# Optimization experiments

Measured on AMD Instinct MI355X. Metric: run time of the kernel, lower is better.

## Reference

```python
import jax, jax.numpy as jnp
import numpy as np

F_DIM = 128
H_DIM = 128
T_DIM = H_DIM // 4          # 32
D = H_DIM + T_DIM           # 160, block hidden dim
N_NODES = 100000
N_EDGES = 800000
N_LAYERS = 2
LN_EPS = 1e-5


def _layernorm(x, g, b):
    m = jnp.mean(x, axis=-1, keepdims=True)
    v = jnp.mean(jnp.square(x - m), axis=-1, keepdims=True)
    return (x - m) * jax.lax.rsqrt(v + LN_EPS) * g + b


def setup_inputs() -> dict:
    key = jax.random.key(0)
    ks = jax.random.split(key, 24)
    p = lambda k, shape: jax.random.normal(k, shape, dtype=jnp.float32) * 0.05
    inp = {
        "node_features": jax.random.normal(ks[0], (N_NODES, F_DIM), dtype=jnp.float32),
        "edge_index": jax.random.randint(ks[1], (2, N_EDGES), 0, N_NODES, dtype=jnp.int32),
        "edge_weights": jax.random.uniform(ks[2], (N_EDGES,), dtype=jnp.float32),
        "time_steps": jax.random.uniform(ks[3], (N_NODES, 1), dtype=jnp.float32),
        # node encoder: Linear(F,H) + LN(H)
        "w_enc": p(ks[4], (H_DIM, F_DIM)), "b_enc": jnp.zeros((H_DIM,)),
        "g_enc": jnp.ones((H_DIM,)), "be_enc": jnp.zeros((H_DIM,)),
        # time encoder: Linear(1,T) + LN(T)
        "w_time": p(ks[5], (T_DIM, 1)), "b_time": jnp.zeros((T_DIM,)),
        "g_time": jnp.ones((T_DIM,)), "be_time": jnp.zeros((T_DIM,)),
        # per-layer block params (stacked over layers)
        "wm": p(ks[6], (N_LAYERS, D, 2 * D)), "bm": jnp.zeros((N_LAYERS, D)),
        "gm": jnp.ones((N_LAYERS, D)), "bem": jnp.zeros((N_LAYERS, D)),
        "wu": p(ks[7], (N_LAYERS, D, 2 * D)), "bu": jnp.zeros((N_LAYERS, D)),
        "gu": jnp.ones((N_LAYERS, D)), "beu": jnp.zeros((N_LAYERS, D)),
        "wg": p(ks[8], (N_LAYERS, 1, D)), "bg": jnp.zeros((N_LAYERS, 1)),
        # output projection Linear(D, F)
        "w_out": p(ks[9], (F_DIM, D)), "b_out": jnp.zeros((F_DIM,)),
    }
    return inp


def _block(h, src, dst, w, wm, bm, gm, bem, wu, bu, gu, beu, wg, bg):
    n = h.shape[0]
    # gather endpoints -> per-edge message MLP -> weight -> scatter-add mean
    ecat = jnp.concatenate([h[src], h[dst]], axis=-1)              # [E, 2D]
    em = jax.nn.relu(_layernorm(ecat @ wm.T + bm, gm, bem)) * w[:, None]
    msum = jax.ops.segment_sum(em, dst, num_segments=n)            # [N, D]
    cnt = jax.ops.segment_sum(jnp.ones_like(w), dst, num_segments=n)[:, None]
    valid = (cnt > 0).astype(h.dtype)
    messages = msum / (cnt + 1e-8) * valid
    tw = jax.nn.sigmoid(h @ wg.T + bg)                             # [N, 1]
    h_new = jax.nn.relu(_layernorm(jnp.concatenate([h, messages], axis=-1) @ wu.T + bu, gu, beu))
    return tw * h_new + (1 - tw) * h


def reference(node_features, edge_index, edge_weights, time_steps,
              w_enc, b_enc, g_enc, be_enc, w_time, b_time, g_time, be_time,
              wm, bm, gm, bem, wu, bu, gu, beu, wg, bg, w_out, b_out):
    src, dst = edge_index[0], edge_index[1]
    h = jax.nn.relu(_layernorm(node_features @ w_enc.T + b_enc, g_enc, be_enc))
    t = jax.nn.relu(_layernorm(time_steps @ w_time.T + b_time, g_time, be_time))
    h_t = jnp.concatenate([h, t], axis=-1)                          # [N, D]
    for l in range(N_LAYERS):
        h_t = _block(h_t, src, dst, edge_weights,
                     wm[l], bm[l], gm[l], bem[l],
                     wu[l], bu[l], gu[l], beu[l], wg[l], bg[l])
    out = h_t @ w_out.T + b_out
    # F.normalize(dim=-1), eps=1e-12
    norm = jnp.linalg.norm(out, axis=-1, keepdims=True)
    return out / jnp.maximum(norm, 1e-12)
```

## Files before the change

kernel.cpp:

```cpp
#include <hip/hip_runtime.h>

#define NN 100000
#define NE 800000

typedef _Float16 half8 __attribute__((ext_vector_type(8)));
typedef _Float16 half4 __attribute__((ext_vector_type(4)));
typedef float floatx4 __attribute__((ext_vector_type(4)));

#define LDB(Wf, f) (*(const half8*)&(Wf)[(f) * 512])

__global__ __launch_bounds__(256) void k_zero(float4* __restrict__ p, int n4) {
  int i = blockIdx.x * 256 + threadIdx.x;
  if (i < n4) p[i] = make_float4(0.f, 0.f, 0.f, 0.f);
}

__global__ __launch_bounds__(256) void k_pack(
    const float* __restrict__ w_enc, const float* __restrict__ w_out,
    const float* __restrict__ wu, const float* __restrict__ wm,
    _Float16* __restrict__ WeP, _Float16* __restrict__ WoP,
    _Float16* __restrict__ WuP, _Float16* __restrict__ WpP) {
  int gid = blockIdx.x * 256 + threadIdx.x;
  int fid = gid >> 6, lane = gid & 63;
  int mrow = lane & 15, quad = lane >> 4;
  const float* src; _Float16* dst; int stride, NI, f, g;
  if (fid < 32) {
    f = fid; g = f; src = w_enc; dst = WeP; stride = 128; NI = 8;
  } else if (fid < 72) {
    f = fid - 32; g = f; src = w_out; dst = WoP; stride = 160; NI = 8;
  } else if (fid < 272) {
    f = fid - 72; g = f % 100; src = wu + (f / 100) * 51200; dst = WuP; stride = 320; NI = 10;
  } else {
    f = fid - 272; g = f % 50;
    int l = f / 100, h = (f % 100) / 50;
    src = wm + l * 51200 + h * 160; dst = WpP; stride = 320; NI = 10;
  }
  int kk = g / NI, i = g - kk * NI;
  const float* sp = src + (size_t)(i * 16 + mrow) * stride + kk * 32 + quad * 8;
  float4 f0 = *(const float4*)sp;
  float4 f1 = *(const float4*)(sp + 4);
  half8 v = {(_Float16)f0.x, (_Float16)f0.y, (_Float16)f0.z, (_Float16)f0.w,
             (_Float16)f1.x, (_Float16)f1.y, (_Float16)f1.z, (_Float16)f1.w};
  *(half8*)&dst[(size_t)(f * 64 + lane) * 8] = v;
}

__global__ __launch_bounds__(256) void k_count_i(const int* __restrict__ ei,
                                                 int* __restrict__ cnti) {
  int e = blockIdx.x * 256 + threadIdx.x;
  atomicAdd(&cnti[ei[NE + e]], 1);
}

__global__ __launch_bounds__(256) void k_scan1(const int* __restrict__ cnti,
                                               int* __restrict__ off,
                                               int* __restrict__ bsum) {
  __shared__ int sh[256];
  const int t = threadIdx.x;
  const int i = blockIdx.x * 256 + t;
  int v = (i < NN) ? cnti[i] : 0;
  sh[t] = v;
  __syncthreads();
  for (int d = 1; d < 256; d <<= 1) {
    int add = (t >= d) ? sh[t - d] : 0;
    __syncthreads();
    sh[t] += add;
    __syncthreads();
  }
  if (i < NN) off[i] = sh[t] - v;
  if (t == 255) bsum[blockIdx.x] = sh[255];
}

__global__ __launch_bounds__(512) void k_scan2(const int* __restrict__ bsum,
                                               int* __restrict__ bsum2) {
  __shared__ int sh[512];
  const int t = threadIdx.x;
  int v = (t < 391) ? bsum[t] : 0;
  sh[t] = v;
  __syncthreads();
  for (int d = 1; d < 512; d <<= 1) {
    int add = (t >= d) ? sh[t - d] : 0;
    __syncthreads();
    sh[t] += add;
    __syncthreads();
  }
  if (t < 391) bsum2[t] = sh[t] - v;
}

__global__ __launch_bounds__(256) void k_scan3(int* __restrict__ off,
                                               const int* __restrict__ bsum2,
                                               int* __restrict__ cursor) {
  const int i = blockIdx.x * 256 + threadIdx.x;
  if (i < NN) {
    int o = off[i] + bsum2[blockIdx.x];
    off[i] = o;
    cursor[i] = o;
  }
  if (i == 0) off[NN] = NE;
}

__global__ __launch_bounds__(256) void k_scatter(const int* __restrict__ ei,
                                                 const float* __restrict__ ew,
                                                 int* __restrict__ cursor,
                                                 int2* __restrict__ selist) {
  int e = blockIdx.x * 256 + threadIdx.x;
  int dst = ei[NE + e];
  int pos = atomicAdd(&cursor[dst], 1);
  selist[pos] = make_int2(ei[e], __float_as_int(ew[e]));
}

__device__ __forceinline__ half8 cvt8(const float* p) {
  float4 f0 = *(const float4*)p;
  float4 f1 = *(const float4*)(p + 4);
  half8 a = {(_Float16)f0.x, (_Float16)f0.y, (_Float16)f0.z, (_Float16)f0.w,
             (_Float16)f1.x, (_Float16)f1.y, (_Float16)f1.z, (_Float16)f1.w};
  return a;
}

__device__ __forceinline__ void write_h16_wave(_Float16* __restrict__ h16,
                                               const _Float16* tile, int n0,
                                               int w, int lane) {
#pragma unroll
  for (int u = 0; u < 5; ++u) {
    int c = lane + u * 64;
    int row = c / 20, col = (c - row * 20) * 8;
    int node = n0 + w * 16 + row;
    if (node < NN)
      *(half8*)&h16[(size_t)node * 160 + col] = *(const half8*)&tile[(w * 16 + row) * 168 + col];
  }
}

__device__ __forceinline__ void phase2_proj(
    const _Float16* __restrict__ WpP, const float* __restrict__ bm,
    _Float16* __restrict__ P, const _Float16* tile,
    int lane, int w, int mrow, int quad, int n0) {
#pragma unroll 1
  for (int half_ = 0; half_ < 2; ++half_) {
    const _Float16* Wf = WpP + half_ * 25600 + lane * 8;
    floatx4 acc2[10];
#pragma unroll
    for (int i = 0; i < 10; ++i) acc2[i] = (floatx4)0.f;
#pragma unroll
    for (int kk = 0; kk < 5; ++kk) {
      half8 a = *(const half8*)&tile[(w * 16 + mrow) * 168 + kk * 32 + quad * 8];
#pragma unroll
      for (int i = 0; i < 10; ++i) {
        half8 b = LDB(Wf, kk * 10 + i);
        acc2[i] = __builtin_amdgcn_mfma_f32_16x16x32_f16(a, b, acc2[i], 0, 0, 0);
      }
    }
#pragma unroll
    for (int r = 0; r < 4; ++r) {
      const int row = quad * 4 + r;
      const int node = n0 + w * 16 + row;
      if (node < NN) {
        _Float16* prow = &P[(size_t)node * 320 + half_ * 160];
#pragma unroll
        for (int i = 0; i < 10; ++i) {
          int jj = i * 16 + mrow;
          prow[jj] = (_Float16)(acc2[i][r] + (half_ ? bm[jj] : 0.f));
        }
      }
    }
  }
}

__global__ __launch_bounds__(128, 4) void k_encode_proj(
    const float* __restrict__ x, const float* __restrict__ tsp,
    const _Float16* __restrict__ WeP,
    const float* __restrict__ b_enc, const float* __restrict__ g_enc,
    const float* __restrict__ be_enc,
    const float* __restrict__ w_time, const float* __restrict__ b_time,
    const float* __restrict__ g_time, const float* __restrict__ be_time,
    const _Float16* __restrict__ WpP, const float* __restrict__ bm,
    _Float16* __restrict__ h16, _Float16* __restrict__ P) {
  __shared__ _Float16 tile[32 * 168];
  const int t = threadIdx.x;
  const int lane = t & 63, w = t >> 6;
  const int mrow = lane & 15, quad = lane >> 4;
  const int n0 = blockIdx.x * 32;
  int arow = n0 + w * 16 + mrow; if (arow > NN - 1) arow = NN - 1;
  const float* xrow = x + (size_t)arow * 128;
  half8 areg[4];
#pragma unroll
  for (int kt = 0; kt < 4; ++kt) areg[kt] = cvt8(&xrow[kt * 32 + quad * 8]);
  float mw = 0.f, mb = 0.f;
  for (int d = 0; d < 32; ++d) { mw += w_time[d]; mb += b_time[d]; }
  mw *= (1.f / 32.f); mb *= (1.f / 32.f);
  float A = 0.f, B = 0.f, C = 0.f;
  for (int d = 0; d < 32; ++d) {
    float a = w_time[d] - mw, c = b_time[d] - mb;
    A = fmaf(a, a, A); B = fmaf(a, c, B); C = fmaf(c, c, C);
  }
  A *= (1.f / 32.f); B *= (1.f / 32.f); C *= (1.f / 32.f);
  floatx4 acc[8];
#pragma unroll
  for (int i = 0; i < 8; ++i) acc[i] = (floatx4)0.f;
  const _Float16* Wf = WeP + lane * 8;
#pragma unroll
  for (int kk = 0; kk < 4; ++kk) {
    half8 a = areg[kk];
#pragma unroll
    for (int i = 0; i < 8; ++i) {
      half8 b = LDB(Wf, kk * 8 + i);
      acc[i] = __builtin_amdgcn_mfma_f32_16x16x32_f16(a, b, acc[i], 0, 0, 0);
    }
  }
#pragma unroll
  for (int r = 0; r < 4; ++r) {
    const int row = quad * 4 + r;
    float v[8], s = 0.f, ss = 0.f;
#pragma unroll
    for (int i = 0; i < 8; ++i) {
      v[i] = acc[i][r] + b_enc[i * 16 + mrow];
      s += v[i]; ss = fmaf(v[i], v[i], ss);
    }
#pragma unroll
    for (int off = 1; off < 16; off <<= 1) { s += __shfl_xor(s, off); ss += __shfl_xor(ss, off); }
    const float m = s * (1.f / 128.f);
    const float rs = rsqrtf(ss * (1.f / 128.f) - m * m + 1e-5f);
#pragma unroll
    for (int i = 0; i < 8; ++i) {
      int j = i * 16 + mrow;
      tile[(w * 16 + row) * 168 + j] =
          (_Float16)fmaxf(fmaf((v[i] - m) * rs, g_enc[j], be_enc[j]), 0.f);
    }
  }
#pragma unroll
  for (int rr = 0; rr < 8; ++rr) {
    int q = lane + rr * 64;
    int nn = q >> 5, d = q & 31;
    int node = n0 + w * 16 + nn;
    int nodec = (node > NN - 1) ? NN - 1 : node;
    float tsv = tsp[nodec];
    float mt = fmaf(mw, tsv, mb);
    float rst = rsqrtf(fmaf(fmaf(A, tsv, 2.f * B), tsv, C) + 1e-5f);
    float vv = fmaf(w_time[d], tsv, b_time[d]);
    float y = fmaxf(fmaf((vv - mt) * rst, g_time[d], be_time[d]), 0.f);
    tile[(w * 16 + nn) * 168 + 128 + d] = (_Float16)y;
  }
  write_h16_wave(h16, tile, n0, w, lane);
  phase2_proj(WpP, bm, P, tile, lane, w, mrow, quad, n0);
}

__global__ __launch_bounds__(256) void k_edge3(
    const _Float16* __restrict__ P, const int* __restrict__ off,
    const int2* __restrict__ selist,
    const float* __restrict__ gm, const float* __restrict__ bem,
    _Float16* __restrict__ msum16) {
  const int t = threadIdx.x;
  const int jg = t & 31, g = t >> 5;
  const int n = blockIdx.x * 8 + g;
  float gmv[5], bev[5], pdv[5];
#pragma unroll
  for (int i = 0; i < 4; ++i) { gmv[i] = gm[4 * jg + i]; bev[i] = bem[4 * jg + i]; }
  gmv[4] = gm[128 + jg]; bev[4] = bem[128 + jg];
  const _Float16* pd = P + (size_t)n * 320 + 160;
  half4 pdh = *(const half4*)&pd[4 * jg];
  pdv[0] = (float)pdh.x; pdv[1] = (float)pdh.y; pdv[2] = (float)pdh.z; pdv[3] = (float)pdh.w;
  pdv[4] = (float)pd[128 + jg];
  float acc[5] = {0.f, 0.f, 0.f, 0.f, 0.f};
  const int e0 = off[n], e1 = off[n + 1];
  int k = e0;
  for (; k + 1 < e1; k += 2) {
    int2 seA = selist[k], seB = selist[k + 1];
    const _Float16* psA = P + (size_t)seA.x * 320;
    const _Float16* psB = P + (size_t)seB.x * 320;
    const float weA = __int_as_float(seA.y), weB = __int_as_float(seB.y);
    half4 a4 = *(const half4*)&psA[4 * jg];
    half4 b4 = *(const half4*)&psB[4 * jg];
    float a5 = (float)psA[128 + jg], b5 = (float)psB[128 + jg];
    float vA[5], vB[5];
    vA[0] = (float)a4.x + pdv[0]; vA[1] = (float)a4.y + pdv[1];
    vA[2] = (float)a4.z + pdv[2]; vA[3] = (float)a4.w + pdv[3]; vA[4] = a5 + pdv[4];
    vB[0] = (float)b4.x + pdv[0]; vB[1] = (float)b4.y + pdv[1];
    vB[2] = (float)b4.z + pdv[2]; vB[3] = (float)b4.w + pdv[3]; vB[4] = b5 + pdv[4];
    float sA = 0.f, ssA = 0.f, sB = 0.f, ssB = 0.f;
#pragma unroll
    for (int i = 0; i < 5; ++i) {
      sA += vA[i]; ssA = fmaf(vA[i], vA[i], ssA);
      sB += vB[i]; ssB = fmaf(vB[i], vB[i], ssB);
    }
#pragma unroll
    for (int o = 1; o < 32; o <<= 1) {
      sA += __shfl_xor(sA, o); ssA += __shfl_xor(ssA, o);
      sB += __shfl_xor(sB, o); ssB += __shfl_xor(ssB, o);
    }
    const float mA = sA * (1.f / 160.f), mB = sB * (1.f / 160.f);
    const float rsA = rsqrtf(ssA * (1.f / 160.f) - mA * mA + 1e-5f);
    const float rsB = rsqrtf(ssB * (1.f / 160.f) - mB * mB + 1e-5f);
#pragma unroll
    for (int i = 0; i < 5; ++i) {
      acc[i] = fmaf(fmaxf(fmaf((vA[i] - mA) * rsA, gmv[i], bev[i]), 0.f), weA, acc[i]);
      acc[i] = fmaf(fmaxf(fmaf((vB[i] - mB) * rsB, gmv[i], bev[i]), 0.f), weB, acc[i]);
    }
  }
  if (k < e1) {
    int2 se = selist[k];
    const _Float16* ps = P + (size_t)se.x * 320;
    const float we = __int_as_float(se.y);
    half4 s4 = *(const half4*)&ps[4 * jg];
    float v[5], s = 0.f, ss = 0.f;
    v[0] = (float)s4.x + pdv[0]; v[1] = (float)s4.y + pdv[1];
    v[2] = (float)s4.z + pdv[2]; v[3] = (float)s4.w + pdv[3];
    v[4] = (float)ps[128 + jg] + pdv[4];
#pragma unroll
    for (int i = 0; i < 5; ++i) { s += v[i]; ss = fmaf(v[i], v[i], ss); }
#pragma unroll
    for (int o = 1; o < 32; o <<= 1) { s += __shfl_xor(s, o); ss += __shfl_xor(ss, o); }
    const float m = s * (1.f / 160.f);
    const float rs = rsqrtf(ss * (1.f / 160.f) - m * m + 1e-5f);
#pragma unroll
    for (int i = 0; i < 5; ++i)
      acc[i] = fmaf(fmaxf(fmaf((v[i] - m) * rs, gmv[i], bev[i]), 0.f), we, acc[i]);
  }
  const float c = (float)(e1 - e0);
  const float ic = (c > 0.f) ? 1.f / (c + 1e-8f) : 0.f;
  _Float16* orow = msum16 + (size_t)n * 160;
  half4 o4 = {(_Float16)(acc[0] * ic), (_Float16)(acc[1] * ic),
              (_Float16)(acc[2] * ic), (_Float16)(acc[3] * ic)};
  *(half4*)&orow[4 * jg] = o4;
  orow[128 + jg] = (_Float16)(acc[4] * ic);
}

__device__ __forceinline__ void update_phase1(
    const _Float16* __restrict__ h16, const _Float16* __restrict__ msum16,
    const _Float16* __restrict__ WuP, const float* __restrict__ bu,
    const float* __restrict__ gu, const float* __restrict__ beu,
    const float* __restrict__ wg, const float* __restrict__ bg,
    _Float16* tile, int lane, int w, int mrow, int quad, int n0) {
  int arow = n0 + w * 16 + mrow; if (arow > NN - 1) arow = NN - 1;
  const _Float16* hrowp = h16 + (size_t)arow * 160;
  const _Float16* mrowp = msum16 + (size_t)arow * 160;
  half8 areg[10];
#pragma unroll
  for (int kt = 0; kt < 5; ++kt) areg[kt] = *(const half8*)&hrowp[kt * 32 + quad * 8];
#pragma unroll
  for (int kt = 5; kt < 10; ++kt) areg[kt] = *(const half8*)&mrowp[kt * 32 + quad * 8 - 160];
  float gp = 0.f;
#pragma unroll
  for (int kt = 0; kt < 5; ++kt) {
    const int k0 = kt * 32 + quad * 8;
    float4 g0 = *(const float4*)&wg[k0];
    float4 g1 = *(const float4*)&wg[k0 + 4];
    gp = fmaf((float)areg[kt][0], g0.x, gp); gp = fmaf((float)areg[kt][1], g0.y, gp);
    gp = fmaf((float)areg[kt][2], g0.z, gp); gp = fmaf((float)areg[kt][3], g0.w, gp);
    gp = fmaf((float)areg[kt][4], g1.x, gp); gp = fmaf((float)areg[kt][5], g1.y, gp);
    gp = fmaf((float)areg[kt][6], g1.z, gp); gp = fmaf((float)areg[kt][7], g1.w, gp);
  }
  gp += __shfl_xor(gp, 16); gp += __shfl_xor(gp, 32);
  const float twv = 1.f / (1.f + expf(-(gp + bg[0])));
  floatx4 acc[10];
#pragma unroll
  for (int i = 0; i < 10; ++i) acc[i] = (floatx4)0.f;
  const _Float16* Wf = WuP + lane * 8;
#pragma unroll
  for (int kk = 0; kk < 10; ++kk) {
    half8 a = areg[kk];
#pragma unroll
    for (int i = 0; i < 10; ++i) {
      half8 b = LDB(Wf, kk * 10 + i);
      acc[i] = __builtin_amdgcn_mfma_f32_16x16x32_f16(a, b, acc[i], 0, 0, 0);
    }
  }
#pragma unroll
  for (int r = 0; r < 4; ++r) {
    const int row = quad * 4 + r;
    const int node = n0 + w * 16 + row;
    const int nodec = (node > NN - 1) ? NN - 1 : node;
    float v[10], s = 0.f, ss = 0.f;
#pragma unroll
    for (int i = 0; i < 10; ++i) {
      v[i] = acc[i][r] + bu[i * 16 + mrow];
      s += v[i]; ss = fmaf(v[i], v[i], ss);
    }
#pragma unroll
    for (int off = 1; off < 16; off <<= 1) { s += __shfl_xor(s, off); ss += __shfl_xor(ss, off); }
    const float m = s * (1.f / 160.f);
    const float rs = rsqrtf(ss * (1.f / 160.f) - m * m + 1e-5f);
    const float g = __shfl(twv, row);
    const _Float16* hr = h16 + (size_t)nodec * 160;
#pragma unroll
    for (int i = 0; i < 10; ++i) {
      int j = i * 16 + mrow;
      float hnew = fmaxf(fmaf((v[i] - m) * rs, gu[j], beu[j]), 0.f);
      float hold = (float)hr[j];
      tile[(w * 16 + row) * 168 + j] = (_Float16)fmaf(g, hnew - hold, hold);
    }
  }
}

__global__ __launch_bounds__(128, 4) void k_update_proj(
    _Float16* __restrict__ h16, const _Float16* __restrict__ msum16,
    const _Float16* __restrict__ WuP, const float* __restrict__ bu,
    const float* __restrict__ gu, const float* __restrict__ beu,
    const float* __restrict__ wg, const float* __restrict__ bg,
    const _Float16* __restrict__ WpP, const float* __restrict__ bm,
    _Float16* __restrict__ P) {
  __shared__ _Float16 tile[32 * 168];
  const int t = threadIdx.x;
  const int lane = t & 63, w = t >> 6;
  const int mrow = lane & 15, quad = lane >> 4;
  const int n0 = blockIdx.x * 32;
  update_phase1(h16, msum16, WuP, bu, gu, beu, wg, bg, tile, lane, w, mrow, quad, n0);
  write_h16_wave(h16, tile, n0, w, lane);
  phase2_proj(WpP, bm, P, tile, lane, w, mrow, quad, n0);
}

__global__ __launch_bounds__(128, 4) void k_update_out(
    const _Float16* __restrict__ h16, const _Float16* __restrict__ msum16,
    const _Float16* __restrict__ WuP, const float* __restrict__ bu,
    const float* __restrict__ gu, const float* __restrict__ beu,
    const float* __restrict__ wg, const float* __restrict__ bg,
    const _Float16* __restrict__ WoP, const float* __restrict__ b_out,
    float* __restrict__ out) {
  __shared__ _Float16 tile[32 * 168];
  const int t = threadIdx.x;
  const int lane = t & 63, w = t >> 6;
  const int mrow = lane & 15, quad = lane >> 4;
  const int n0 = blockIdx.x * 32;
  update_phase1(h16, msum16, WuP, bu, gu, beu, wg, bg, tile, lane, w, mrow, quad, n0);
  floatx4 acc2[8];
#pragma unroll
  for (int i = 0; i < 8; ++i) acc2[i] = (floatx4)0.f;
  const _Float16* Wf2 = WoP + lane * 8;
#pragma unroll
  for (int kk = 0; kk < 5; ++kk) {
    half8 a = *(const half8*)&tile[(w * 16 + mrow) * 168 + kk * 32 + quad * 8];
#pragma unroll
    for (int i = 0; i < 8; ++i) {
      half8 b = LDB(Wf2, kk * 8 + i);
      acc2[i] = __builtin_amdgcn_mfma_f32_16x16x32_f16(a, b, acc2[i], 0, 0, 0);
    }
  }
#pragma unroll
  for (int r = 0; r < 4; ++r) {
    const int row = quad * 4 + r;
    const int node = n0 + w * 16 + row;
    float v[8], ss = 0.f;
#pragma unroll
    for (int i = 0; i < 8; ++i) {
      v[i] = acc2[i][r] + b_out[i * 16 + mrow];
      ss = fmaf(v[i], v[i], ss);
    }
#pragma unroll
    for (int off = 1; off < 16; off <<= 1) ss += __shfl_xor(ss, off);
    const float inv = 1.f / fmaxf(sqrtf(ss), 1e-12f);
    if (node < NN) {
#pragma unroll
      for (int i = 0; i < 8; ++i)
        out[(size_t)node * 128 + i * 16 + mrow] = v[i] * inv;
    }
  }
}

extern "C" void kernel_launch(void* const* d_in, const int* in_sizes, int n_in,
                              void* d_out, int out_size, void* d_ws, size_t ws_size,
                              hipStream_t stream) {
  (void)in_sizes; (void)n_in; (void)out_size; (void)ws_size;
  const float* x       = (const float*)d_in[0];
  const int*   ei      = (const int*)  d_in[1];
  const float* ew      = (const float*)d_in[2];
  const float* tsp     = (const float*)d_in[3];
  const float* w_enc   = (const float*)d_in[4];
  const float* b_enc   = (const float*)d_in[5];
  const float* g_enc   = (const float*)d_in[6];
  const float* be_enc  = (const float*)d_in[7];
  const float* w_time  = (const float*)d_in[8];
  const float* b_time  = (const float*)d_in[9];
  const float* g_time  = (const float*)d_in[10];
  const float* be_time = (const float*)d_in[11];
  const float* wm      = (const float*)d_in[12];
  const float* bm      = (const float*)d_in[13];
  const float* gm      = (const float*)d_in[14];
  const float* bem     = (const float*)d_in[15];
  const float* wu      = (const float*)d_in[16];
  const float* bu      = (const float*)d_in[17];
  const float* gu      = (const float*)d_in[18];
  const float* beu     = (const float*)d_in[19];
  const float* wg      = (const float*)d_in[20];
  const float* bg      = (const float*)d_in[21];
  const float* w_out   = (const float*)d_in[22];
  const float* b_out   = (const float*)d_in[23];
  float* out = (float*)d_out;

  char* ws = (char*)d_ws;
  _Float16* h16    = (_Float16*)ws;
  _Float16* msum16 = (_Float16*)(ws + 32000000);
  _Float16* P      = (_Float16*)(ws + 64000000);
  _Float16* WuP16  = (_Float16*)(ws + 128000000);
  _Float16* WoP16  = (_Float16*)(ws + 128204800);
  char* ob = (char*)d_out;
  _Float16* WpP16 = (_Float16*)ob;
  _Float16* WeP16 = (_Float16*)(ob + 204800);
  int* off    = (int*)(ob + 237568);
  int* cnti   = (int*)(ob + 637584);
  int* cursor = (int*)(ob + 1037584);
  int* bsum   = (int*)(ob + 1437584);
  int* bsum2  = (int*)(ob + 1439152);
  int2* selist = (int2*)(ob + 1440720);

  k_zero<<<dim3(98), dim3(256), 0, stream>>>((float4*)cnti, 25000);
  k_pack<<<dim3(118), dim3(256), 0, stream>>>(w_enc, w_out, wu, wm,
                                              WeP16, WoP16, WuP16, WpP16);
  k_count_i<<<dim3(3125), dim3(256), 0, stream>>>(ei, cnti);
  k_scan1<<<dim3(391), dim3(256), 0, stream>>>(cnti, off, bsum);
  k_scan2<<<dim3(1), dim3(512), 0, stream>>>(bsum, bsum2);
  k_scan3<<<dim3(391), dim3(256), 0, stream>>>(off, bsum2, cursor);
  k_scatter<<<dim3(3125), dim3(256), 0, stream>>>(ei, ew, cursor, selist);

  k_encode_proj<<<dim3(3125), dim3(128), 0, stream>>>(
      x, tsp, WeP16, b_enc, g_enc, be_enc, w_time, b_time, g_time, be_time,
      WpP16, bm, h16, P);
  k_edge3<<<dim3(12500), dim3(256), 0, stream>>>(P, off, selist, gm, bem, msum16);
  k_update_proj<<<dim3(3125), dim3(128), 0, stream>>>(
      h16, msum16, WuP16, bu, gu, beu, wg, bg,
      WpP16 + 51200, bm + 160, P);
  k_edge3<<<dim3(12500), dim3(256), 0, stream>>>(P, off, selist, gm + 160, bem + 160, msum16);
  k_update_out<<<dim3(3125), dim3(128), 0, stream>>>(
      h16, msum16, WuP16 + 51200, bu + 160, gu + 160, beu + 160, wg + 160, bg + 1,
      WoP16, b_out, out);
}
```

Measured before the change: 555.0 us.

## Double-buffer weight fragments and shrink node kernels to one wave per block

The three node-level MFMA kernels now run 16 nodes per 64-thread block instead of 32 nodes per 128 threads, so each block is a single wave and uses half the shared tile. Their GEMM loops are rewritten to software-pipeline the B-fragment loads in groups of 4 or 5 with ping-pong register buffers, also prefetching the next GEMM's first weight group across phases. A-operand loads are streamed per k-step instead of being held all at once. This targets global-load latency stalls on the weights, at the cost of more live registers and dropped bounds checks, which are safe only because NN divides evenly by 16.

```diff
diff --git a/kernel.cpp b/kernel.cpp
--- a/kernel.cpp
+++ b/kernel.cpp
@@ -114,55 +114,68 @@
   return a;
 }
 
+__device__ __forceinline__ void ldg5(half8 d[5], const _Float16* Wf, int g) {
+#pragma unroll
+  for (int ii = 0; ii < 5; ++ii) d[ii] = LDB(Wf, g * 5 + ii);
+}
+__device__ __forceinline__ void ldg4(half8 d[4], const _Float16* Wf, int g) {
+#pragma unroll
+  for (int ii = 0; ii < 4; ++ii) d[ii] = LDB(Wf, g * 4 + ii);
+}
+
 __device__ __forceinline__ void write_h16_wave(_Float16* __restrict__ h16,
                                                const _Float16* tile, int n0,
-                                               int w, int lane) {
+                                               int lane) {
 #pragma unroll
   for (int u = 0; u < 5; ++u) {
     int c = lane + u * 64;
     int row = c / 20, col = (c - row * 20) * 8;
-    int node = n0 + w * 16 + row;
-    if (node < NN)
-      *(half8*)&h16[(size_t)node * 160 + col] = *(const half8*)&tile[(w * 16 + row) * 168 + col];
+    *(half8*)&h16[(size_t)(n0 + row) * 160 + col] = *(const half8*)&tile[row * 168 + col];
   }
 }
 
 __device__ __forceinline__ void phase2_proj(
     const _Float16* __restrict__ WpP, const float* __restrict__ bm,
-    _Float16* __restrict__ P, const _Float16* tile,
-    int lane, int w, int mrow, int quad, int n0) {
-#pragma unroll 1
+    _Float16* __restrict__ P, const _Float16* tile, half8 bA[5], half8 bB[5],
+    int lane, int mrow, int quad, int n0) {
+#pragma unroll
   for (int half_ = 0; half_ < 2; ++half_) {
     const _Float16* Wf = WpP + half_ * 25600 + lane * 8;
+    const _Float16* Wfn = WpP + 25600 + lane * 8;
     floatx4 acc2[10];
 #pragma unroll
     for (int i = 0; i < 10; ++i) acc2[i] = (floatx4)0.f;
-#pragma unroll
-    for (int kk = 0; kk < 5; ++kk) {
-      half8 a = *(const half8*)&tile[(w * 16 + mrow) * 168 + kk * 32 + quad * 8];
-#pragma unroll
-      for (int i = 0; i < 10; ++i) {
-        half8 b = LDB(Wf, kk * 10 + i);
-        acc2[i] = __builtin_amdgcn_mfma_f32_16x16x32_f16(a, b, acc2[i], 0, 0, 0);
+    half8 a_cur = *(const half8*)&tile[mrow * 168 + quad * 8];
+#pragma unroll
+    for (int g = 0; g < 10; ++g) {
+      half8* bc = (g & 1) ? bB : bA;
+      half8* bn = (g & 1) ? bA : bB;
+      if (g + 1 < 10) ldg5(bn, Wf, g + 1);
+      else if (half_ == 0) ldg5(bn, Wfn, 0);
+      half8 a_use = a_cur;
+      if ((g & 1) && g < 9) {
+        int kk1 = (g + 1) >> 1;
+        a_cur = *(const half8*)&tile[mrow * 168 + kk1 * 32 + quad * 8];
       }
+      const int ib = (g & 1) * 5;
+#pragma unroll
+      for (int ii = 0; ii < 5; ++ii)
+        acc2[ib + ii] = __builtin_amdgcn_mfma_f32_16x16x32_f16(a_use, bc[ii], acc2[ib + ii], 0, 0, 0);
     }
 #pragma unroll
     for (int r = 0; r < 4; ++r) {
       const int row = quad * 4 + r;
-      const int node = n0 + w * 16 + row;
-      if (node < NN) {
-        _Float16* prow = &P[(size_t)node * 320 + half_ * 160];
-#pragma unroll
-        for (int i = 0; i < 10; ++i) {
-          int jj = i * 16 + mrow;
-          prow[jj] = (_Float16)(acc2[i][r] + (half_ ? bm[jj] : 0.f));
-        }
+      _Float16* prow = &P[(size_t)(n0 + row) * 320 + half_ * 160];
+#pragma unroll
+      for (int i = 0; i < 10; ++i) {
+        int jj = i * 16 + mrow;
+        prow[jj] = (_Float16)(acc2[i][r] + (half_ ? bm[jj] : 0.f));
       }
     }
   }
 }
 
-__global__ __launch_bounds__(128, 4) void k_encode_proj(
+__global__ __launch_bounds__(64, 4) void k_encode_proj(
     const float* __restrict__ x, const float* __restrict__ tsp,
     const _Float16* __restrict__ WeP,
     const float* __restrict__ b_enc, const float* __restrict__ g_enc,
@@ -171,16 +184,14 @@
     const float* __restrict__ g_time, const float* __restrict__ be_time,
     const _Float16* __restrict__ WpP, const float* __restrict__ bm,
     _Float16* __restrict__ h16, _Float16* __restrict__ P) {
-  __shared__ _Float16 tile[32 * 168];
-  const int t = threadIdx.x;
-  const int lane = t & 63, w = t >> 6;
+  __shared__ _Float16 tile[16 * 168];
+  const int lane = threadIdx.x;
   const int mrow = lane & 15, quad = lane >> 4;
-  const int n0 = blockIdx.x * 32;
-  int arow = n0 + w * 16 + mrow; if (arow > NN - 1) arow = NN - 1;
-  const float* xrow = x + (size_t)arow * 128;
-  half8 areg[4];
-#pragma unroll
-  for (int kt = 0; kt < 4; ++kt) areg[kt] = cvt8(&xrow[kt * 32 + quad * 8]);
+  const int n0 = blockIdx.x * 16;
+  const float* xrow = x + (size_t)(n0 + mrow) * 128;
+  const _Float16* Wf = WeP + lane * 8;
+  half8 cA[4], cB[4];
+  ldg4(cA, Wf, 0);
   float mw = 0.f, mb = 0.f;
   for (int d = 0; d < 32; ++d) { mw += w_time[d]; mb += b_time[d]; }
   mw *= (1.f / 32.f); mb *= (1.f / 32.f);
@@ -193,16 +204,24 @@
   floatx4 acc[8];
 #pragma unroll
   for (int i = 0; i < 8; ++i) acc[i] = (floatx4)0.f;
-  const _Float16* Wf = WeP + lane * 8;
-#pragma unroll
-  for (int kk = 0; kk < 4; ++kk) {
-    half8 a = areg[kk];
-#pragma unroll
-    for (int i = 0; i < 8; ++i) {
-      half8 b = LDB(Wf, kk * 8 + i);
-      acc[i] = __builtin_amdgcn_mfma_f32_16x16x32_f16(a, b, acc[i], 0, 0, 0);
-    }
-  }
+  half8 a_cur = cvt8(&xrow[quad * 8]);
+#pragma unroll
+  for (int g = 0; g < 8; ++g) {
+    half8* bc = (g & 1) ? cB : cA;
+    half8* bn = (g & 1) ? cA : cB;
+    if (g + 1 < 8) ldg4(bn, Wf, g + 1);
+    half8 a_use = a_cur;
+    if ((g & 1) && g < 7) {
+      int kk1 = (g + 1) >> 1;
+      a_cur = cvt8(&xrow[kk1 * 32 + quad * 8]);
+    }
+    const int ib = (g & 1) * 4;
+#pragma unroll
+    for (int ii = 0; ii < 4; ++ii)
+      acc[ib + ii] = __builtin_amdgcn_mfma_f32_16x16x32_f16(a_use, bc[ii], acc[ib + ii], 0, 0, 0);
+  }
+  half8 bA[5], bB[5];
+  ldg5(bA, WpP + lane * 8, 0);
 #pragma unroll
   for (int r = 0; r < 4; ++r) {
     const int row = quad * 4 + r;
@@ -219,7 +238,7 @@
 #pragma unroll
     for (int i = 0; i < 8; ++i) {
       int j = i * 16 + mrow;
-      tile[(w * 16 + row) * 168 + j] =
+      tile[row * 168 + j] =
           (_Float16)fmaxf(fmaf((v[i] - m) * rs, g_enc[j], be_enc[j]), 0.f);
     }
   }
@@ -227,17 +246,15 @@
   for (int rr = 0; rr < 8; ++rr) {
     int q = lane + rr * 64;
     int nn = q >> 5, d = q & 31;
-    int node = n0 + w * 16 + nn;
-    int nodec = (node > NN - 1) ? NN - 1 : node;
-    float tsv = tsp[nodec];
+    float tsv = tsp[n0 + nn];
     float mt = fmaf(mw, tsv, mb);
     float rst = rsqrtf(fmaf(fmaf(A, tsv, 2.f * B), tsv, C) + 1e-5f);
     float vv = fmaf(w_time[d], tsv, b_time[d]);
     float y = fmaxf(fmaf((vv - mt) * rst, g_time[d], be_time[d]), 0.f);
-    tile[(w * 16 + nn) * 168 + 128 + d] = (_Float16)y;
-  }
-  write_h16_wave(h16, tile, n0, w, lane);
-  phase2_proj(WpP, bm, P, tile, lane, w, mrow, quad, n0);
+    tile[nn * 168 + 128 + d] = (_Float16)y;
+  }
+  write_h16_wave(h16, tile, n0, lane);
+  phase2_proj(WpP, bm, P, tile, bA, bB, lane, mrow, quad, n0);
 }
 
 __global__ __launch_bounds__(256) void k_edge3(
@@ -325,46 +342,50 @@
     const _Float16* __restrict__ WuP, const float* __restrict__ bu,
     const float* __restrict__ gu, const float* __restrict__ beu,
     const float* __restrict__ wg, const float* __restrict__ bg,
-    _Float16* tile, int lane, int w, int mrow, int quad, int n0) {
-  int arow = n0 + w * 16 + mrow; if (arow > NN - 1) arow = NN - 1;
-  const _Float16* hrowp = h16 + (size_t)arow * 160;
-  const _Float16* mrowp = msum16 + (size_t)arow * 160;
-  half8 areg[10];
-#pragma unroll
-  for (int kt = 0; kt < 5; ++kt) areg[kt] = *(const half8*)&hrowp[kt * 32 + quad * 8];
-#pragma unroll
-  for (int kt = 5; kt < 10; ++kt) areg[kt] = *(const half8*)&mrowp[kt * 32 + quad * 8 - 160];
+    const _Float16* __restrict__ WpPf,
+    _Float16* tile, half8 bA[5], half8 bB[5],
+    int lane, int mrow, int quad, int n0) {
+  const _Float16* h0 = h16 + (size_t)(n0 + mrow) * 160;
+  const _Float16* ms0 = msum16 + (size_t)(n0 + mrow) * 160;
+  const _Float16* Wf = WuP + lane * 8;
+  ldg5(bA, Wf, 0);
   float gp = 0.f;
 #pragma unroll
   for (int kt = 0; kt < 5; ++kt) {
-    const int k0 = kt * 32 + quad * 8;
-    float4 g0 = *(const float4*)&wg[k0];
-    float4 g1 = *(const float4*)&wg[k0 + 4];
-    gp = fmaf((float)areg[kt][0], g0.x, gp); gp = fmaf((float)areg[kt][1], g0.y, gp);
-    gp = fmaf((float)areg[kt][2], g0.z, gp); gp = fmaf((float)areg[kt][3], g0.w, gp);
-    gp = fmaf((float)areg[kt][4], g1.x, gp); gp = fmaf((float)areg[kt][5], g1.y, gp);
-    gp = fmaf((float)areg[kt][6], g1.z, gp); gp = fmaf((float)areg[kt][7], g1.w, gp);
+    half8 ha = *(const half8*)&h0[kt * 32 + quad * 8];
+    float4 g0 = *(const float4*)&wg[kt * 32 + quad * 8];
+    float4 g1 = *(const float4*)&wg[kt * 32 + quad * 8 + 4];
+    gp = fmaf((float)ha[0], g0.x, gp); gp = fmaf((float)ha[1], g0.y, gp);
+    gp = fmaf((float)ha[2], g0.z, gp); gp = fmaf((float)ha[3], g0.w, gp);
+    gp = fmaf((float)ha[4], g1.x, gp); gp = fmaf((float)ha[5], g1.y, gp);
+    gp = fmaf((float)ha[6], g1.z, gp); gp = fmaf((float)ha[7], g1.w, gp);
   }
   gp += __shfl_xor(gp, 16); gp += __shfl_xor(gp, 32);
   const float twv = 1.f / (1.f + expf(-(gp + bg[0])));
   floatx4 acc[10];
 #pragma unroll
   for (int i = 0; i < 10; ++i) acc[i] = (floatx4)0.f;
-  const _Float16* Wf = WuP + lane * 8;
-#pragma unroll
-  for (int kk = 0; kk < 10; ++kk) {
-    half8 a = areg[kk];
-#pragma unroll
-    for (int i = 0; i < 10; ++i) {
-      half8 b = LDB(Wf, kk * 10 + i);
-      acc[i] = __builtin_amdgcn_mfma_f32_16x16x32_f16(a, b, acc[i], 0, 0, 0);
-    }
-  }
+  half8 a_cur = *(const half8*)&h0[quad * 8];
+#pragma unroll
+  for (int g = 0; g < 20; ++g) {
+    half8* bc = (g & 1) ? bB : bA;
+    half8* bn = (g & 1) ? bA : bB;
+    if (g + 1 < 20) ldg5(bn, Wf, g + 1);
+    half8 a_use = a_cur;
+    if ((g & 1) && g < 19) {
+      int kk1 = (g + 1) >> 1;
+      const _Float16* ap = (kk1 < 5) ? h0 + kk1 * 32 : ms0 + (kk1 - 5) * 32;
+      a_cur = *(const half8*)&ap[quad * 8];
+    }
+    const int ib = (g & 1) * 5;
+#pragma unroll
+    for (int ii = 0; ii < 5; ++ii)
+      acc[ib + ii] = __builtin_amdgcn_mfma_f32_16x16x32_f16(a_use, bc[ii], acc[ib + ii], 0, 0, 0);
+  }
+  ldg5(bA, WpPf, 0);
 #pragma unroll
   for (int r = 0; r < 4; ++r) {
     const int row = quad * 4 + r;
-    const int node = n0 + w * 16 + row;
-    const int nodec = (node > NN - 1) ? NN - 1 : node;
     float v[10], s = 0.f, ss = 0.f;
 #pragma unroll
     for (int i = 0; i < 10; ++i) {
@@ -376,64 +397,75 @@
     const float m = s * (1.f / 160.f);
     const float rs = rsqrtf(ss * (1.f / 160.f) - m * m + 1e-5f);
     const float g = __shfl(twv, row);
-    const _Float16* hr = h16 + (size_t)nodec * 160;
+    const _Float16* hr = h16 + (size_t)(n0 + row) * 160;
 #pragma unroll
     for (int i = 0; i < 10; ++i) {
       int j = i * 16 + mrow;
       float hnew = fmaxf(fmaf((v[i] - m) * rs, gu[j], beu[j]), 0.f);
       float hold = (float)hr[j];
-      tile[(w * 16 + row) * 168 + j] = (_Float16)fmaf(g, hnew - hold, hold);
-    }
-  }
-}
-
-__global__ __launch_bounds__(128, 4) void k_update_proj(
+      tile[row * 168 + j] = (_Float16)fmaf(g, hnew - hold, hold);
+    }
+  }
+}
+
+__global__ __launch_bounds__(64, 4) void k_update_proj(
     _Float16* __restrict__ h16, const _Float16* __restrict__ msum16,
     const _Float16* __restrict__ WuP, const float* __restrict__ bu,
     const float* __restrict__ gu, const float* __restrict__ beu,
     const float* __restrict__ wg, const float* __restrict__ bg,
     const _Float16* __restrict__ WpP, const float* __restrict__ bm,
     _Float16* __restrict__ P) {
-  __shared__ _Float16 tile[32 * 168];
-  const int t = threadIdx.x;
-  const int lane = t & 63, w = t >> 6;
+  __shared__ _Float16 tile[16 * 168];
+  const int lane = threadIdx.x;
   const int mrow = lane & 15, quad = lane >> 4;
-  const int n0 = blockIdx.x * 32;
-  update_phase1(h16, msum16, WuP, bu, gu, beu, wg, bg, tile, lane, w, mrow, quad, n0);
-  write_h16_wave(h16, tile, n0, w, lane);
-  phase2_proj(WpP, bm, P, tile, lane, w, mrow, quad, n0);
-}
-
-__global__ __launch_bounds__(128, 4) void k_update_out(
+  const int n0 = blockIdx.x * 16;
+  half8 bA[5], bB[5];
+  update_phase1(h16, msum16, WuP, bu, gu, beu, wg, bg,
+                WpP + lane * 8, tile, bA, bB, lane, mrow, quad, n0);
+  write_h16_wave(h16, tile, n0, lane);
+  phase2_proj(WpP, bm, P, tile, bA, bB, lane, mrow, quad, n0);
+}
+
+__global__ __launch_bounds__(64, 4) void k_update_out(
     const _Float16* __restrict__ h16, const _Float16* __restrict__ msum16,
     const _Float16* __restrict__ WuP, const float* __restrict__ bu,
     const float* __restrict__ gu, const float* __restrict__ beu,
     const float* __restrict__ wg, const float* __restrict__ bg,
     const _Float16* __restrict__ WoP, const float* __restrict__ b_out,
     float* __restrict__ out) {
-  __shared__ _Float16 tile[32 * 168];
-  const int t = threadIdx.x;
-  const int lane = t & 63, w = t >> 6;
+  __shared__ _Float16 tile[16 * 168];
+  const int lane = threadIdx.x;
   const int mrow = lane & 15, quad = lane >> 4;
-  const int n0 = blockIdx.x * 32;
-  update_phase1(h16, msum16, WuP, bu, gu, beu, wg, bg, tile, lane, w, mrow, quad, n0);
+  const int n0 = blockIdx.x * 16;
+  half8 bA[5], bB[5];
+  update_phase1(h16, msum16, WuP, bu, gu, beu, wg, bg,
+                WoP + lane * 8, tile, bA, bB, lane, mrow, quad, n0);
+  const _Float16* Wf2 = WoP + lane * 8;
+  half8 cA[4], cB[4];
+#pragma unroll
+  for (int ii = 0; ii < 4; ++ii) cA[ii] = bA[ii];
   floatx4 acc2[8];
 #pragma unroll
   for (int i = 0; i < 8; ++i) acc2[i] = (floatx4)0.f;
-  const _Float16* Wf2 = WoP + lane * 8;
-#pragma unroll
-  for (int kk = 0; kk < 5; ++kk) {
-    half8 a = *(const half8*)&tile[(w * 16 + mrow) * 168 + kk * 32 + quad * 8];
-#pragma unroll
-    for (int i = 0; i < 8; ++i) {
-      half8 b = LDB(Wf2, kk * 8 + i);
-      acc2[i] = __builtin_amdgcn_mfma_f32_16x16x32_f16(a, b, acc2[i], 0, 0, 0);
-    }
+  half8 a_cur = *(const half8*)&tile[mrow * 168 + quad * 8];
+#pragma unroll
+  for (int g = 0; g < 10; ++g) {
+    half8* bc = (g & 1) ? cB : cA;
+    half8* bn = (g & 1) ? cA : cB;
+    if (g + 1 < 10) ldg4(bn, Wf2, g + 1);
+    half8 a_use = a_cur;
+    if ((g & 1) && g < 9) {
+      int kk1 = (g + 1) >> 1;
+      a_cur = *(const half8*)&tile[mrow * 168 + kk1 * 32 + quad * 8];
+    }
+    const int ib = (g & 1) * 4;
+#pragma unroll
+    for (int ii = 0; ii < 4; ++ii)
+      acc2[ib + ii] = __builtin_amdgcn_mfma_f32_16x16x32_f16(a_use, bc[ii], acc2[ib + ii], 0, 0, 0);
   }
 #pragma unroll
   for (int r = 0; r < 4; ++r) {
     const int row = quad * 4 + r;
-    const int node = n0 + w * 16 + row;
     float v[8], ss = 0.f;
 #pragma unroll
     for (int i = 0; i < 8; ++i) {
@@ -443,11 +475,9 @@
 #pragma unroll
     for (int off = 1; off < 16; off <<= 1) ss += __shfl_xor(ss, off);
     const float inv = 1.f / fmaxf(sqrtf(ss), 1e-12f);
-    if (node < NN) {
-#pragma unroll
-      for (int i = 0; i < 8; ++i)
-        out[(size_t)node * 128 + i * 16 + mrow] = v[i] * inv;
-    }
+#pragma unroll
+    for (int i = 0; i < 8; ++i)
+      out[(size_t)(n0 + row) * 128 + i * 16 + mrow] = v[i] * inv;
   }
 }
 
@@ -506,15 +536,15 @@
   k_scan3<<<dim3(391), dim3(256), 0, stream>>>(off, bsum2, cursor);
   k_scatter<<<dim3(3125), dim3(256), 0, stream>>>(ei, ew, cursor, selist);
 
-  k_encode_proj<<<dim3(3125), dim3(128), 0, stream>>>(
+  k_encode_proj<<<dim3(6250), dim3(64), 0, stream>>>(
       x, tsp, WeP16, b_enc, g_enc, be_enc, w_time, b_time, g_time, be_time,
       WpP16, bm, h16, P);
   k_edge3<<<dim3(12500), dim3(256), 0, stream>>>(P, off, selist, gm, bem, msum16);
-  k_update_proj<<<dim3(3125), dim3(128), 0, stream>>>(
+  k_update_proj<<<dim3(6250), dim3(64), 0, stream>>>(
       h16, msum16, WuP16, bu, gu, beu, wg, bg,
       WpP16 + 51200, bm + 160, P);
   k_edge3<<<dim3(12500), dim3(256), 0, stream>>>(P, off, selist, gm + 160, bem + 160, msum16);
-  k_update_out<<<dim3(3125), dim3(128), 0, stream>>>(
+  k_update_out<<<dim3(6250), dim3(64), 0, stream>>>(
       h16, msum16, WuP16 + 51200, bu + 160, gu + 160, beu + 160, wg + 160, bg + 1,
       WoP16, b_out, out);
 }
```

Measured after the change: 554.3 us. About the same (-0.1%).
